# Kernel tuning notes

Hardware: AMD Instinct MI355X
Metric: run time of the kernel (lower is better)

Reference implementation:

```python
import jax, jax.numpy as jnp
import numpy as np

B, A, H, V, L = 8192, 128, 256, 64, 20


def setup_inputs() -> dict:
    key = jax.random.key(0)
    ks = jax.random.split(key, 9)
    s = lambda k, sh: jax.random.normal(k, sh, dtype=jnp.float32) * 0.05
    return {
        "attrVector": jax.random.normal(ks[0], (B, A), dtype=jnp.float32),
        "W_a": s(ks[1], (H, A)), "b_a": s(ks[2], (H,)),
        "W_ih": s(ks[3], (4 * H, V)), "W_hh": s(ks[4], (4 * H, H)),
        "b_ih": s(ks[5], (4 * H,)), "b_hh": s(ks[6], (4 * H,)),
        "W_v": s(ks[7], (V, H)), "b_v": s(ks[8], (V,)),
    }


def _lstm_step(x, h, c, W_ih, W_hh, b_ih, b_hh):
    # PyTorch LSTM gate order: input, forget, cell(g), output
    gates = x @ W_ih.T + b_ih + h @ W_hh.T + b_hh  # [B, 4H]
    i, f, g, o = jnp.split(gates, 4, axis=-1)
    c_new = jax.nn.sigmoid(f) * c + jax.nn.sigmoid(i) * jnp.tanh(g)
    h_new = jax.nn.sigmoid(o) * jnp.tanh(c_new)
    return h_new, c_new


def reference(attrVector, W_a, b_a, W_ih, W_hh, b_ih, b_hh, W_v, b_v):
    batch = attrVector.shape[0]
    dt = attrVector.dtype
    # attr2hidden -> initial hidden state; cell state zeros (init_hidden)
    h = attrVector @ W_a.T + b_a                      # [B, H]
    c = jnp.zeros_like(h)
    # start-token step (all-zeros embedding)
    x0 = jnp.zeros((batch, V), dtype=dt)
    h, c = _lstm_step(x0, h, c, W_ih, W_hh, b_ih, b_hh)

    keys = jax.random.split(jax.random.key(42), L)

    def step(carry, k):
        h, c, slp, plp, ep = carry
        logits = h @ W_v.T + b_v                      # [B, V]
        logp = jax.nn.log_softmax(logits, axis=-1)
        plp = plp + jnp.sum(jnp.exp(logp) * logp, axis=-1)  # negative entropy
        ch = jax.random.categorical(k, logits, axis=-1)     # [B] int sample
        lp = jnp.take_along_axis(logp, ch[:, None], axis=-1)[:, 0]
        slp = slp + lp
        ep = ep * jnp.exp(lp)
        x = jax.nn.one_hot(ch, V, dtype=dt)
        h2, c2 = _lstm_step(x, h, c, W_ih, W_hh, b_ih, b_hh)
        return (h2, c2, slp, plp, ep), ch

    zeros = jnp.zeros((batch,), dtype=dt)
    ones = jnp.ones((batch,), dtype=dt)
    (_, _, slp, plp, ep), msgs = jax.lax.scan(step, (h, c, zeros, zeros, ones), keys)
    message = msgs.T.astype(jnp.int64) if msgs.dtype != jnp.int64 else msgs.T  # [B, L]
    return message, slp, plp, ep
```

## Files before the change

kernel.cpp:

```cpp
#include <hip/hip_runtime.h>
#include <stdint.h>

#define BATCH 8192
#define ADIM 128
#define HDIM 256
#define VDIM 64
#define NSTEP 20
#define TB 16
#define TBP 20

typedef union { float4 v; float f[4]; } F4;

__device__ __forceinline__ uint32_t rotl32(uint32_t x, uint32_t d) {
  return (x << d) | (x >> (32u - d));
}
__device__ __forceinline__ void tf4(uint32_t& x0, uint32_t& x1, int r0, int r1, int r2, int r3) {
  x0 += x1; x1 = rotl32(x1, r0); x1 ^= x0;
  x0 += x1; x1 = rotl32(x1, r1); x1 ^= x0;
  x0 += x1; x1 = rotl32(x1, r2); x1 ^= x0;
  x0 += x1; x1 = rotl32(x1, r3); x1 ^= x0;
}
__device__ __forceinline__ void threefry2x32(uint32_t k0, uint32_t k1, uint32_t x0, uint32_t x1,
                                             uint32_t& o0, uint32_t& o1) {
  uint32_t k2 = k0 ^ k1 ^ 0x1BD11BDAu;
  x0 += k0; x1 += k1;
  tf4(x0, x1, 13, 15, 26, 6);  x0 += k1; x1 += k2 + 1u;
  tf4(x0, x1, 17, 29, 16, 24); x0 += k2; x1 += k0 + 2u;
  tf4(x0, x1, 13, 15, 26, 6);  x0 += k0; x1 += k1 + 3u;
  tf4(x0, x1, 17, 29, 16, 24); x0 += k1; x1 += k2 + 4u;
  tf4(x0, x1, 13, 15, 26, 6);  x0 += k2; x1 += k0 + 5u;
  o0 = x0; o1 = x1;
}

__device__ __forceinline__ float sigm(float x) { return 1.0f / (1.0f + expf(-x)); }

__global__ void prep_kernel(const float* __restrict__ Whh, const float* __restrict__ Wv,
                            const float* __restrict__ Wa, const float* __restrict__ Wih,
                            float* __restrict__ ws) {
  int n = blockIdx.x * blockDim.x + threadIdx.x;
  int stride = gridDim.x * blockDim.x;
  float* WhhT = ws;
  float* WvT  = ws + 262144;
  float* WaT  = ws + 278528;
  float* WihT = ws + 311296;
  for (int i = n; i < 256 * 1024; i += stride) { int k = i >> 10, r = i & 1023; WhhT[i] = Whh[r * 256 + k]; }
  for (int i = n; i < 256 * 64;   i += stride) { int k = i >> 6,  v = i & 63;   WvT[i]  = Wv[v * 256 + k]; }
  for (int i = n; i < 128 * 256;  i += stride) { int k = i >> 8,  u = i & 255;  WaT[i]  = Wa[u * 128 + k]; }
  for (int i = n; i < 64 * 1024;  i += stride) { int v = i >> 10, r = i & 1023; WihT[i] = Wih[r * 64 + v]; }
}

__global__ __launch_bounds__(256, 2) void sender_main(
    const float* __restrict__ attr, const float* __restrict__ b_a,
    const float* __restrict__ b_ih, const float* __restrict__ b_hh,
    const float* __restrict__ b_v,
    const float* __restrict__ WhhT, const float* __restrict__ WvT,
    const float* __restrict__ WaT, const float* __restrict__ WihT,
    float* __restrict__ out) {
  __shared__ float h_s[HDIM][TBP];
  __shared__ float attr_s[ADIM][TBP];
  __shared__ float slp_s[TB], plp_s[TB], ep_s[TB];

  const int tid = threadIdx.x;
  const int tb = tid >> 6;
  const int tu = tid & 63;
  const int tb4 = tb << 2;
  const int tu4 = tu << 2;
  const int b0 = blockIdx.x * TB;

  if (tid < TB) { slp_s[tid] = 0.0f; plp_s[tid] = 0.0f; ep_s[tid] = 1.0f; }

  {
    int r = tid >> 5;
    int cm = (tid & 31) << 2;
    #pragma unroll
    for (int pass = 0; pass < 2; ++pass) {
      int row = r + (pass << 3);
      F4 vv; vv.v = *(const float4*)&attr[(size_t)(b0 + row) * ADIM + cm];
      attr_s[cm + 0][row] = vv.f[0];
      attr_s[cm + 1][row] = vv.f[1];
      attr_s[cm + 2][row] = vv.f[2];
      attr_s[cm + 3][row] = vv.f[3];
    }
  }
  __syncthreads();

  {
    float acc[4][4];
    #pragma unroll
    for (int a = 0; a < 4; ++a)
      #pragma unroll
      for (int j = 0; j < 4; ++j) acc[a][j] = 0.0f;
    for (int k = 0; k < ADIM; ++k) {
      F4 av; av.v = *(const float4*)&attr_s[k][tb4];
      F4 wv; wv.v = *(const float4*)&WaT[(k << 8) + tu4];
      #pragma unroll
      for (int db = 0; db < 4; ++db)
        #pragma unroll
        for (int j = 0; j < 4; ++j) acc[db][j] = fmaf(av.f[db], wv.f[j], acc[db][j]);
    }
    F4 ba; ba.v = *(const float4*)&b_a[tu4];
    #pragma unroll
    for (int db = 0; db < 4; ++db)
      #pragma unroll
      for (int j = 0; j < 4; ++j) h_s[tu4 + j][tb4 + db] = acc[db][j] + ba.f[j];
  }
  __syncthreads();

  float c_r[4][4];
  #pragma unroll
  for (int db = 0; db < 4; ++db)
    #pragma unroll
    for (int j = 0; j < 4; ++j) c_r[db][j] = 0.0f;

  F4 bg[4];
  #pragma unroll
  for (int g = 0; g < 4; ++g) {
    F4 bi; bi.v = *(const float4*)&b_ih[(g << 8) + tu4];
    F4 bh; bh.v = *(const float4*)&b_hh[(g << 8) + tu4];
    #pragma unroll
    for (int j = 0; j < 4; ++j) bg[g].f[j] = bi.f[j] + bh.f[j];
  }
  const float bv = b_v[tu];

  {
    float ga[4][4][4];
    #pragma unroll
    for (int db = 0; db < 4; ++db)
      #pragma unroll
      for (int g = 0; g < 4; ++g)
        #pragma unroll
        for (int j = 0; j < 4; ++j) ga[db][g][j] = 0.0f;
    for (int k = 0; k < HDIM; ++k) {
      F4 hv; hv.v = *(const float4*)&h_s[k][tb4];
      const float* wr = WhhT + (k << 10) + tu4;
      F4 w0, w1, w2, w3;
      w0.v = *(const float4*)(wr);
      w1.v = *(const float4*)(wr + 256);
      w2.v = *(const float4*)(wr + 512);
      w3.v = *(const float4*)(wr + 768);
      #pragma unroll
      for (int db = 0; db < 4; ++db) {
        float hd = hv.f[db];
        #pragma unroll
        for (int j = 0; j < 4; ++j) {
          ga[db][0][j] = fmaf(hd, w0.f[j], ga[db][0][j]);
          ga[db][1][j] = fmaf(hd, w1.f[j], ga[db][1][j]);
          ga[db][2][j] = fmaf(hd, w2.f[j], ga[db][2][j]);
          ga[db][3][j] = fmaf(hd, w3.f[j], ga[db][3][j]);
        }
      }
    }
    __syncthreads();
    #pragma unroll
    for (int db = 0; db < 4; ++db)
      #pragma unroll
      for (int j = 0; j < 4; ++j) {
        float gi = ga[db][0][j] + bg[0].f[j];
        float gf = ga[db][1][j] + bg[1].f[j];
        float gg = ga[db][2][j] + bg[2].f[j];
        float go = ga[db][3][j] + bg[3].f[j];
        float cn = sigm(gf) * c_r[db][j] + sigm(gi) * tanhf(gg);
        float hn = sigm(go) * tanhf(cn);
        c_r[db][j] = cn;
        h_s[tu4 + j][tb4 + db] = hn;
      }
    __syncthreads();
  }

  for (int l = 0; l < NSTEP; ++l) {
    uint32_t kl0, kl1;
    threefry2x32(0u, 42u, 0u, (uint32_t)l, kl0, kl1);

    const bool last = (l == NSTEP - 1);
    float la[4] = {0.0f, 0.0f, 0.0f, 0.0f};
    float ga[4][4][4];
    #pragma unroll
    for (int db = 0; db < 4; ++db)
      #pragma unroll
      for (int g = 0; g < 4; ++g)
        #pragma unroll
        for (int j = 0; j < 4; ++j) ga[db][g][j] = 0.0f;

    if (!last) {
      for (int k = 0; k < HDIM; ++k) {
        F4 hv; hv.v = *(const float4*)&h_s[k][tb4];
        float wv = WvT[(k << 6) | tu];
        const float* wr = WhhT + (k << 10) + tu4;
        F4 w0, w1, w2, w3;
        w0.v = *(const float4*)(wr);
        w1.v = *(const float4*)(wr + 256);
        w2.v = *(const float4*)(wr + 512);
        w3.v = *(const float4*)(wr + 768);
        #pragma unroll
        for (int db = 0; db < 4; ++db) {
          float hd = hv.f[db];
          la[db] = fmaf(hd, wv, la[db]);
          #pragma unroll
          for (int j = 0; j < 4; ++j) {
            ga[db][0][j] = fmaf(hd, w0.f[j], ga[db][0][j]);
            ga[db][1][j] = fmaf(hd, w1.f[j], ga[db][1][j]);
            ga[db][2][j] = fmaf(hd, w2.f[j], ga[db][2][j]);
            ga[db][3][j] = fmaf(hd, w3.f[j], ga[db][3][j]);
          }
        }
      }
    } else {
      for (int k = 0; k < HDIM; ++k) {
        F4 hv; hv.v = *(const float4*)&h_s[k][tb4];
        float wv = WvT[(k << 6) | tu];
        #pragma unroll
        for (int db = 0; db < 4; ++db) la[db] = fmaf(hv.f[db], wv, la[db]);
      }
    }

    int ch[4];
    #pragma unroll 1
    for (int db = 0; db < 4; ++db) {
      float x = la[db] + bv;
      float m = x;
      #pragma unroll
      for (int o = 32; o > 0; o >>= 1) m = fmaxf(m, __shfl_xor(m, o));
      float e = expf(x - m);
      float s = e;
      #pragma unroll
      for (int o = 32; o > 0; o >>= 1) s += __shfl_xor(s, o);
      float lse = logf(s);
      float logp = x - m - lse;
      float p = expf(logp);
      float pe = p * logp;
      #pragma unroll
      for (int o = 32; o > 0; o >>= 1) pe += __shfl_xor(pe, o);
      uint32_t idx = ((uint32_t)(b0 + tb4 + db) << 6) | (uint32_t)tu;
      uint32_t r0, r1;
      threefry2x32(kl0, kl1, 0u, idx, r0, r1);
      uint32_t bits = r0 ^ r1;
      float f01 = __uint_as_float((bits >> 9) | 0x3f800000u) - 1.0f;
      const float TINY = 1.17549435e-38f;
      float u = fmaxf(TINY, f01 + TINY);
      float gn = -logf(-logf(u));
      float y = gn + x;
      float by = y; int bi = tu;
      #pragma unroll
      for (int o = 32; o > 0; o >>= 1) {
        float oy = __shfl_xor(by, o);
        int oi = __shfl_xor(bi, o);
        if (oy > by || (oy == by && oi < bi)) { by = oy; bi = oi; }
      }
      ch[db] = bi;
      float lp = __shfl(logp, bi, 64);
      if (tu == 0) {
        int bb = tb4 + db;
        slp_s[bb] += lp;
        plp_s[bb] += pe;
        ep_s[bb] *= expf(lp);
        out[(size_t)(b0 + bb) * NSTEP + l] = (float)bi;
      }
    }

    if (!last) {
      __syncthreads();
      #pragma unroll 1
      for (int db = 0; db < 4; ++db) {
        const float* wi = WihT + (ch[db] << 10) + tu4;
        F4 wi0, wi1, wi2, wi3;
        wi0.v = *(const float4*)(wi);
        wi1.v = *(const float4*)(wi + 256);
        wi2.v = *(const float4*)(wi + 512);
        wi3.v = *(const float4*)(wi + 768);
        #pragma unroll
        for (int j = 0; j < 4; ++j) {
          float gi = ga[db][0][j] + wi0.f[j] + bg[0].f[j];
          float gf = ga[db][1][j] + wi1.f[j] + bg[1].f[j];
          float gg = ga[db][2][j] + wi2.f[j] + bg[2].f[j];
          float go = ga[db][3][j] + wi3.f[j] + bg[3].f[j];
          float cn = sigm(gf) * c_r[db][j] + sigm(gi) * tanhf(gg);
          float hn = sigm(go) * tanhf(cn);
          c_r[db][j] = cn;
          h_s[tu4 + j][tb4 + db] = hn;
        }
      }
      __syncthreads();
    }
  }

  __syncthreads();
  if (tid < TB) {
    int bb = b0 + tid;
    out[(size_t)BATCH * NSTEP + bb]             = slp_s[tid];
    out[(size_t)BATCH * NSTEP + BATCH + bb]     = plp_s[tid];
    out[(size_t)BATCH * NSTEP + 2 * BATCH + bb] = ep_s[tid];
  }
}

extern "C" void kernel_launch(void* const* d_in, const int* in_sizes, int n_in,
                              void* d_out, int out_size, void* d_ws, size_t ws_size,
                              hipStream_t stream) {
  const float* attr = (const float*)d_in[0];
  const float* W_a  = (const float*)d_in[1];
  const float* b_a  = (const float*)d_in[2];
  const float* W_ih = (const float*)d_in[3];
  const float* W_hh = (const float*)d_in[4];
  const float* b_ih = (const float*)d_in[5];
  const float* b_hh = (const float*)d_in[6];
  const float* W_v  = (const float*)d_in[7];
  const float* b_v  = (const float*)d_in[8];
  float* ws = (float*)d_ws;

  prep_kernel<<<256, 256, 0, stream>>>(W_hh, W_v, W_a, W_ih, ws);
  sender_main<<<BATCH / TB, 256, 0, stream>>>(
      attr, b_a, b_ih, b_hh, b_v,
      ws, ws + 262144, ws + 278528, ws + 311296,
      (float*)d_out);
}
```

Before: 1.765 ms.

## Remap thread tiling so each wavefront covers distinct hidden units for all samples

Changes the thread-to-work mapping: each wavefront now owns a 64-unit slice of the hidden dimension across all 16 samples, where before each wavefront owned 4 samples across all units. Weight loads for W_hh become per-wavefront disjoint and coalesced within 16-lane groups, with broadcasts of h across lane groups. The sampling part keeps a per-wavefront sample mapping, so chosen tokens are exchanged through shared memory. It also adds unroll-2 pragmas on the k loops. The cost is an extra LDS read of h per k and a shared-memory exchange of choices.

```diff
diff --git a/kernel.cpp b/kernel.cpp
--- a/kernel.cpp
+++ b/kernel.cpp
@@ -59,12 +59,16 @@
   __shared__ float h_s[HDIM][TBP];
   __shared__ float attr_s[ADIM][TBP];
   __shared__ float slp_s[TB], plp_s[TB], ep_s[TB];
+  __shared__ int ch_s[TB];
 
   const int tid = threadIdx.x;
-  const int tb = tid >> 6;
-  const int tu = tid & 63;
-  const int tb4 = tb << 2;
-  const int tu4 = tu << 2;
+  const int w = tid >> 6;
+  const int lane = tid & 63;
+  const int uu = lane & 15;
+  const int sq = lane >> 4;
+  const int u4 = (w << 6) + (uu << 2);
+  const int s4 = sq << 2;
+  const int w4 = w << 2;
   const int b0 = blockIdx.x * TB;
 
   if (tid < TB) { slp_s[tid] = 0.0f; plp_s[tid] = 0.0f; ep_s[tid] = 1.0f; }
@@ -87,82 +91,83 @@
   {
     float acc[4][4];
     #pragma unroll
-    for (int a = 0; a < 4; ++a)
-      #pragma unroll
-      for (int j = 0; j < 4; ++j) acc[a][j] = 0.0f;
+    for (int s = 0; s < 4; ++s)
+      #pragma unroll
+      for (int j = 0; j < 4; ++j) acc[s][j] = 0.0f;
     for (int k = 0; k < ADIM; ++k) {
-      F4 av; av.v = *(const float4*)&attr_s[k][tb4];
-      F4 wv; wv.v = *(const float4*)&WaT[(k << 8) + tu4];
-      #pragma unroll
-      for (int db = 0; db < 4; ++db)
-        #pragma unroll
-        for (int j = 0; j < 4; ++j) acc[db][j] = fmaf(av.f[db], wv.f[j], acc[db][j]);
-    }
-    F4 ba; ba.v = *(const float4*)&b_a[tu4];
-    #pragma unroll
-    for (int db = 0; db < 4; ++db)
-      #pragma unroll
-      for (int j = 0; j < 4; ++j) h_s[tu4 + j][tb4 + db] = acc[db][j] + ba.f[j];
+      F4 av; av.v = *(const float4*)&attr_s[k][s4];
+      F4 wv; wv.v = *(const float4*)&WaT[(k << 8) + u4];
+      #pragma unroll
+      for (int s = 0; s < 4; ++s)
+        #pragma unroll
+        for (int j = 0; j < 4; ++j) acc[s][j] = fmaf(av.f[s], wv.f[j], acc[s][j]);
+    }
+    F4 ba; ba.v = *(const float4*)&b_a[u4];
+    #pragma unroll
+    for (int s = 0; s < 4; ++s)
+      #pragma unroll
+      for (int j = 0; j < 4; ++j) h_s[u4 + j][s4 + s] = acc[s][j] + ba.f[j];
   }
   __syncthreads();
 
   float c_r[4][4];
   #pragma unroll
-  for (int db = 0; db < 4; ++db)
-    #pragma unroll
-    for (int j = 0; j < 4; ++j) c_r[db][j] = 0.0f;
+  for (int s = 0; s < 4; ++s)
+    #pragma unroll
+    for (int j = 0; j < 4; ++j) c_r[s][j] = 0.0f;
 
   F4 bg[4];
   #pragma unroll
   for (int g = 0; g < 4; ++g) {
-    F4 bi; bi.v = *(const float4*)&b_ih[(g << 8) + tu4];
-    F4 bh; bh.v = *(const float4*)&b_hh[(g << 8) + tu4];
+    F4 bi; bi.v = *(const float4*)&b_ih[(g << 8) + u4];
+    F4 bh; bh.v = *(const float4*)&b_hh[(g << 8) + u4];
     #pragma unroll
     for (int j = 0; j < 4; ++j) bg[g].f[j] = bi.f[j] + bh.f[j];
   }
-  const float bv = b_v[tu];
+  const float bv = b_v[lane];
 
   {
     float ga[4][4][4];
     #pragma unroll
-    for (int db = 0; db < 4; ++db)
+    for (int s = 0; s < 4; ++s)
       #pragma unroll
       for (int g = 0; g < 4; ++g)
         #pragma unroll
-        for (int j = 0; j < 4; ++j) ga[db][g][j] = 0.0f;
+        for (int j = 0; j < 4; ++j) ga[s][g][j] = 0.0f;
+    #pragma unroll 2
     for (int k = 0; k < HDIM; ++k) {
-      F4 hv; hv.v = *(const float4*)&h_s[k][tb4];
-      const float* wr = WhhT + (k << 10) + tu4;
+      F4 hv; hv.v = *(const float4*)&h_s[k][s4];
+      const float* wr = WhhT + (k << 10) + u4;
       F4 w0, w1, w2, w3;
       w0.v = *(const float4*)(wr);
       w1.v = *(const float4*)(wr + 256);
       w2.v = *(const float4*)(wr + 512);
       w3.v = *(const float4*)(wr + 768);
       #pragma unroll
-      for (int db = 0; db < 4; ++db) {
-        float hd = hv.f[db];
+      for (int s = 0; s < 4; ++s) {
+        float hd = hv.f[s];
         #pragma unroll
         for (int j = 0; j < 4; ++j) {
-          ga[db][0][j] = fmaf(hd, w0.f[j], ga[db][0][j]);
-          ga[db][1][j] = fmaf(hd, w1.f[j], ga[db][1][j]);
-          ga[db][2][j] = fmaf(hd, w2.f[j], ga[db][2][j]);
-          ga[db][3][j] = fmaf(hd, w3.f[j], ga[db][3][j]);
+          ga[s][0][j] = fmaf(hd, w0.f[j], ga[s][0][j]);
+          ga[s][1][j] = fmaf(hd, w1.f[j], ga[s][1][j]);
+          ga[s][2][j] = fmaf(hd, w2.f[j], ga[s][2][j]);
+          ga[s][3][j] = fmaf(hd, w3.f[j], ga[s][3][j]);
         }
       }
     }
     __syncthreads();
     #pragma unroll
-    for (int db = 0; db < 4; ++db)
+    for (int s = 0; s < 4; ++s)
       #pragma unroll
       for (int j = 0; j < 4; ++j) {
-        float gi = ga[db][0][j] + bg[0].f[j];
-        float gf = ga[db][1][j] + bg[1].f[j];
-        float gg = ga[db][2][j] + bg[2].f[j];
-        float go = ga[db][3][j] + bg[3].f[j];
-        float cn = sigm(gf) * c_r[db][j] + sigm(gi) * tanhf(gg);
+        float gi = ga[s][0][j] + bg[0].f[j];
+        float gf = ga[s][1][j] + bg[1].f[j];
+        float gg = ga[s][2][j] + bg[2].f[j];
+        float go = ga[s][3][j] + bg[3].f[j];
+        float cn = sigm(gf) * c_r[s][j] + sigm(gi) * tanhf(gg);
         float hn = sigm(go) * tanhf(cn);
-        c_r[db][j] = cn;
-        h_s[tu4 + j][tb4 + db] = hn;
+        c_r[s][j] = cn;
+        h_s[u4 + j][s4 + s] = hn;
       }
     __syncthreads();
   }
@@ -175,45 +180,47 @@
     float la[4] = {0.0f, 0.0f, 0.0f, 0.0f};
     float ga[4][4][4];
     #pragma unroll
-    for (int db = 0; db < 4; ++db)
+    for (int s = 0; s < 4; ++s)
       #pragma unroll
       for (int g = 0; g < 4; ++g)
         #pragma unroll
-        for (int j = 0; j < 4; ++j) ga[db][g][j] = 0.0f;
+        for (int j = 0; j < 4; ++j) ga[s][g][j] = 0.0f;
 
     if (!last) {
+      #pragma unroll 2
       for (int k = 0; k < HDIM; ++k) {
-        F4 hv; hv.v = *(const float4*)&h_s[k][tb4];
-        float wv = WvT[(k << 6) | tu];
-        const float* wr = WhhT + (k << 10) + tu4;
+        F4 hv; hv.v = *(const float4*)&h_s[k][s4];
+        F4 hl; hl.v = *(const float4*)&h_s[k][w4];
+        float wv = WvT[(k << 6) | lane];
+        const float* wr = WhhT + (k << 10) + u4;
         F4 w0, w1, w2, w3;
         w0.v = *(const float4*)(wr);
         w1.v = *(const float4*)(wr + 256);
         w2.v = *(const float4*)(wr + 512);
         w3.v = *(const float4*)(wr + 768);
         #pragma unroll
-        for (int db = 0; db < 4; ++db) {
-          float hd = hv.f[db];
-          la[db] = fmaf(hd, wv, la[db]);
+        for (int s = 0; s < 4; ++s) {
+          la[s] = fmaf(hl.f[s], wv, la[s]);
+          float hd = hv.f[s];
           #pragma unroll
           for (int j = 0; j < 4; ++j) {
-            ga[db][0][j] = fmaf(hd, w0.f[j], ga[db][0][j]);
-            ga[db][1][j] = fmaf(hd, w1.f[j], ga[db][1][j]);
-            ga[db][2][j] = fmaf(hd, w2.f[j], ga[db][2][j]);
-            ga[db][3][j] = fmaf(hd, w3.f[j], ga[db][3][j]);
+            ga[s][0][j] = fmaf(hd, w0.f[j], ga[s][0][j]);
+            ga[s][1][j] = fmaf(hd, w1.f[j], ga[s][1][j]);
+            ga[s][2][j] = fmaf(hd, w2.f[j], ga[s][2][j]);
+            ga[s][3][j] = fmaf(hd, w3.f[j], ga[s][3][j]);
           }
         }
       }
     } else {
+      #pragma unroll 2
       for (int k = 0; k < HDIM; ++k) {
-        F4 hv; hv.v = *(const float4*)&h_s[k][tb4];
-        float wv = WvT[(k << 6) | tu];
-        #pragma unroll
-        for (int db = 0; db < 4; ++db) la[db] = fmaf(hv.f[db], wv, la[db]);
-      }
-    }
-
-    int ch[4];
+        F4 hl; hl.v = *(const float4*)&h_s[k][w4];
+        float wv = WvT[(k << 6) | lane];
+        #pragma unroll
+        for (int s = 0; s < 4; ++s) la[s] = fmaf(hl.f[s], wv, la[s]);
+      }
+    }
+
     #pragma unroll 1
     for (int db = 0; db < 4; ++db) {
       float x = la[db] + bv;
@@ -230,7 +237,7 @@
       float pe = p * logp;
       #pragma unroll
       for (int o = 32; o > 0; o >>= 1) pe += __shfl_xor(pe, o);
-      uint32_t idx = ((uint32_t)(b0 + tb4 + db) << 6) | (uint32_t)tu;
+      uint32_t idx = ((uint32_t)(b0 + w4 + db) << 6) | (uint32_t)lane;
       uint32_t r0, r1;
       threefry2x32(kl0, kl1, 0u, idx, r0, r1);
       uint32_t bits = r0 ^ r1;
@@ -239,17 +246,17 @@
       float u = fmaxf(TINY, f01 + TINY);
       float gn = -logf(-logf(u));
       float y = gn + x;
-      float by = y; int bi = tu;
+      float by = y; int bi = lane;
       #pragma unroll
       for (int o = 32; o > 0; o >>= 1) {
         float oy = __shfl_xor(by, o);
         int oi = __shfl_xor(bi, o);
         if (oy > by || (oy == by && oi < bi)) { by = oy; bi = oi; }
       }
-      ch[db] = bi;
       float lp = __shfl(logp, bi, 64);
-      if (tu == 0) {
-        int bb = tb4 + db;
+      if (lane == 0) {
+        int bb = w4 + db;
+        ch_s[bb] = bi;
         slp_s[bb] += lp;
         plp_s[bb] += pe;
         ep_s[bb] *= expf(lp);
@@ -260,8 +267,8 @@
     if (!last) {
       __syncthreads();
       #pragma unroll 1
-      for (int db = 0; db < 4; ++db) {
-        const float* wi = WihT + (ch[db] << 10) + tu4;
+      for (int s = 0; s < 4; ++s) {
+        const float* wi = WihT + (ch_s[s4 + s] << 10) + u4;
         F4 wi0, wi1, wi2, wi3;
         wi0.v = *(const float4*)(wi);
         wi1.v = *(const float4*)(wi + 256);
@@ -269,14 +276,14 @@
         wi3.v = *(const float4*)(wi + 768);
         #pragma unroll
         for (int j = 0; j < 4; ++j) {
-          float gi = ga[db][0][j] + wi0.f[j] + bg[0].f[j];
-          float gf = ga[db][1][j] + wi1.f[j] + bg[1].f[j];
-          float gg = ga[db][2][j] + wi2.f[j] + bg[2].f[j];
-          float go = ga[db][3][j] + wi3.f[j] + bg[3].f[j];
-          float cn = sigm(gf) * c_r[db][j] + sigm(gi) * tanhf(gg);
+          float gi = ga[s][0][j] + wi0.f[j] + bg[0].f[j];
+          float gf = ga[s][1][j] + wi1.f[j] + bg[1].f[j];
+          float gg = ga[s][2][j] + wi2.f[j] + bg[2].f[j];
+          float go = ga[s][3][j] + wi3.f[j] + bg[3].f[j];
+          float cn = sigm(gf) * c_r[s][j] + sigm(gi) * tanhf(gg);
           float hn = sigm(go) * tanhf(cn);
-          c_r[db][j] = cn;
-          h_s[tu4 + j][tb4 + db] = hn;
+          c_r[s][j] = cn;
+          h_s[u4 + j][s4 + s] = hn;
         }
       }
       __syncthreads();
@@ -298,10 +305,10 @@
   const float* attr = (const float*)d_in[0];
   const float* W_a  = (const float*)d_in[1];
   const float* b_a  = (const float*)d_in[2];
+  const float* b_ih = (const float*)d_in[5];
+  const float* b_hh = (const float*)d_in[6];
   const float* W_ih = (const float*)d_in[3];
   const float* W_hh = (const float*)d_in[4];
-  const float* b_ih = (const float*)d_in[5];
-  const float* b_hh = (const float*)d_in[6];
   const float* W_v  = (const float*)d_in[7];
   const float* b_v  = (const float*)d_in[8];
   float* ws = (float*)d_ws;
```

Result: slower. 2.175 ms (+23.3%).
